# Kernel tuning notes

Hardware: AMD Instinct MI355X
Metric: run time of the kernel (lower is better)

The kernel has to match this reference:

```python
import jax, jax.numpy as jnp
import numpy as np

B = 500000
DT = 1.0

def _first_principles_A(dt):
    A = np.eye(8, dtype=np.float32)
    for i in range(4):
        A[i, i + 4] = dt
    return jnp.asarray(A)

def setup_inputs() -> dict:
    key = jax.random.key(0)
    k1, k2 = jax.random.split(key)
    # bbox-like state: keep positions/sizes positive so Q heuristic is sensible
    x = jax.random.uniform(k1, (B, 8, 1), dtype=jnp.float32, minval=0.1, maxval=1.0)
    P = jax.random.normal(k2, (B, 8, 8), dtype=jnp.float32) * 0.1
    A = _first_principles_A(DT)  # relu/triu leave it unchanged but we apply them anyway
    sigma_p = jnp.float32(0.05)
    sigma_v = jnp.float32(0.00625)
    return {"x": x, "P": P, "A": A, "sigma_p": sigma_p, "sigma_v": sigma_v}

def reference(x, P, A, sigma_p, sigma_v):
    # get_motion_matrix: relu then triu
    Ap = jnp.triu(jax.nn.relu(A))  # (8, 8)
    # x_hat = A @ x
    x_hat = jnp.einsum('ij,bjk->bik', Ap, x)  # (B, 8, 1)
    # process-noise heuristic: diag proportional to bbox h, w (x[:,2,0], x[:,3,0])
    h = x[:, 2, 0]
    w = x[:, 3, 0]
    xp, yp = h * sigma_p, w * sigma_p
    xv, yv = h * sigma_v, w * sigma_v
    diag = jnp.stack([xp, yp, xp, yp, xv, yv, xv, yv], axis=-1)  # (B, 8)
    Q = jnp.square(diag)[:, :, None] * jnp.eye(8, dtype=x.dtype)  # (B, 8, 8) diagonal
    # P_hat = A P A^T + Q
    P_hat = jnp.einsum('ij,bjk,lk->bil', Ap, P, Ap) + Q
    return (x_hat, P_hat)
```

## Files before the change

kernel.cpp:

```cpp
#include <hip/hip_runtime.h>


#define ROW_STRIDE 12
#define ELEM_STRIDE 100
#define ELEMS_PER_BLOCK 32

__device__ __align__(16) float g_cst[72];

__global__ void kalman_setup_kernel(const float* __restrict__ A,
                                    const float* __restrict__ sigp_ptr,
                                    const float* __restrict__ sigv_ptr)
{
    int t = threadIdx.x;
    if (t < 64) {
        float a = fmaxf(A[t], 0.0f);
        if ((t & 7) < (t >> 3)) a = 0.0f;
        g_cst[t] = a;
    }
    if (t < 8) g_cst[64 + t] = (t < 4) ? sigp_ptr[0] : sigv_ptr[0];
}

__global__ __launch_bounds__(256) void kalman_predict_kernel(
    const float* __restrict__ x,
    const float* __restrict__ P,
    float* __restrict__ x_hat,
    float* __restrict__ P_hat,
    int B)
{
    __shared__ float lds_m[ELEMS_PER_BLOCK * ELEM_STRIDE];

    int tid = blockIdx.x * blockDim.x + threadIdx.x;
    int e = tid >> 3;
    int r = tid & 7;
    int e_l = threadIdx.x >> 3;

    bool valid = (e < B);
    int e_c = valid ? e : (B - 1);

    unsigned poff = (unsigned)e_c * 64u + (unsigned)r * 8u;
    const float4* prow = (const float4*)(P + poff);
    float4 pa = prow[0], pb = prow[1];
    float p[8] = {pa.x, pa.y, pa.z, pa.w, pb.x, pb.y, pb.z, pb.w};

    const float4* xrow = (const float4*)(x + (unsigned)e_c * 8u);
    float4 x0 = xrow[0], x1 = xrow[1];
    float xv[8] = {x0.x, x0.y, x0.z, x0.w, x1.x, x1.y, x1.z, x1.w};

    float ap[64];
#pragma unroll
    for (int t = 0; t < 64; ++t) ap[t] = g_cst[t];

    const float4* arow = (const float4*)(g_cst + r * 8);
    float4 a0 = arow[0], a1 = arow[1];
    float apr[8] = {a0.x, a0.y, a0.z, a0.w, a1.x, a1.y, a1.z, a1.w};

    float sig = g_cst[64 + r];

    float m[8];
#pragma unroll
    for (int l = 0; l < 8; ++l) {
        float s = 0.0f;
#pragma unroll
        for (int k = l; k < 8; ++k) s = fmaf(ap[l * 8 + k], p[k], s);
        m[l] = s;
    }

    float* slot = lds_m + e_l * ELEM_STRIDE + r * ROW_STRIDE;
    ((float4*)slot)[0] = make_float4(m[0], m[1], m[2], m[3]);
    ((float4*)(slot + 4))[0] = make_float4(m[4], m[5], m[6], m[7]);

    asm volatile("s_waitcnt lgkmcnt(0)" ::: "memory");

    float hv = (r & 1) ? xv[3] : xv[2];
    float q = hv * sig;
    q = q * q;

    float xh = 0.0f;
#pragma unroll
    for (int j = 0; j < 8; ++j) xh = fmaf(apr[j], xv[j], xh);

    float out[8];
#pragma unroll
    for (int l = 0; l < 8; ++l) out[l] = (l == r) ? q : 0.0f;

    const float* ebase = lds_m + e_l * ELEM_STRIDE;
#pragma unroll
    for (int j = 0; j < 8; ++j) {
        const float4* mr = (const float4*)(ebase + j * ROW_STRIDE);
        float4 ma = mr[0], mb = mr[1];
        float mj[8] = {ma.x, ma.y, ma.z, ma.w, mb.x, mb.y, mb.z, mb.w};
#pragma unroll
        for (int l = 0; l < 8; ++l) out[l] = fmaf(apr[j], mj[l], out[l]);
    }

    if (valid) {
        x_hat[(unsigned)e * 8u + r] = xh;
        float4* po = (float4*)(P_hat + poff);
        po[0] = make_float4(out[0], out[1], out[2], out[3]);
        po[1] = make_float4(out[4], out[5], out[6], out[7]);
    }
}

extern "C" void kernel_launch(void* const* d_in, const int* in_sizes, int n_in,
                              void* d_out, int out_size, void* d_ws, size_t ws_size,
                              hipStream_t stream) {
    const float* x  = (const float*)d_in[0];
    const float* P  = (const float*)d_in[1];
    const float* A  = (const float*)d_in[2];
    const float* sp = (const float*)d_in[3];
    const float* sv = (const float*)d_in[4];

    int B = in_sizes[0] / 8;
    float* x_hat = (float*)d_out;
    float* P_hat = (float*)d_out + (size_t)B * 8;

    kalman_setup_kernel<<<1, 64, 0, stream>>>(A, sp, sv);

    int threads = B * 8;
    int block = 256;
    int grid = (threads + block - 1) / block;
    kalman_predict_kernel<<<grid, block, 0, stream>>>(x, P, x_hat, P_hat, B);
}
```

Measured before the change: 251.7 us.

## Process four elements per thread with hoisted loads and packed triangular constants

Each thread now handles four batch elements instead of one. All P and x loads for those elements are issued up front, before any compute, to raise memory-level parallelism. The grid shrinks by four, and the LDS slot is reused across the iterations. The upper-triangular motion matrix is also stored packed (36 values) alongside the full matrix, cutting per-thread constant loads and register use. The cost is more registers held for the outstanding loads and fewer waves in flight.

```diff
diff --git a/kernel.cpp b/kernel.cpp
--- a/kernel.cpp
+++ b/kernel.cpp
@@ -3,9 +3,10 @@
 
 #define ROW_STRIDE 12
 #define ELEM_STRIDE 100
-#define ELEMS_PER_BLOCK 32
+#define SLOTS 32
+#define EPT 4
 
-__device__ __align__(16) float g_cst[72];
+__device__ __align__(16) float g_cst[112];
 
 __global__ void kalman_setup_kernel(const float* __restrict__ A,
                                     const float* __restrict__ sigp_ptr,
@@ -13,11 +14,16 @@
 {
     int t = threadIdx.x;
     if (t < 64) {
+        int l = t >> 3, k = t & 7;
         float a = fmaxf(A[t], 0.0f);
-        if ((t & 7) < (t >> 3)) a = 0.0f;
-        g_cst[t] = a;
+        if (k < l) a = 0.0f;
+        g_cst[48 + t] = a;
+        if (k >= l) {
+            int off = l * 8 - (l * (l - 1)) / 2;
+            g_cst[off + (k - l)] = a;
+        }
     }
-    if (t < 8) g_cst[64 + t] = (t < 4) ? sigp_ptr[0] : sigv_ptr[0];
+    if (t < 8) g_cst[36 + t] = (t < 4) ? sigp_ptr[0] : sigv_ptr[0];
 }
 
 __global__ __launch_bounds__(256) void kalman_predict_kernel(
@@ -27,77 +33,90 @@
     float* __restrict__ P_hat,
     int B)
 {
-    __shared__ float lds_m[ELEMS_PER_BLOCK * ELEM_STRIDE];
+    __shared__ float lds_m[SLOTS * ELEM_STRIDE];
 
-    int tid = blockIdx.x * blockDim.x + threadIdx.x;
-    int e = tid >> 3;
-    int r = tid & 7;
+    int r   = threadIdx.x & 7;
     int e_l = threadIdx.x >> 3;
+    int eb  = blockIdx.x * (SLOTS * EPT);
 
-    bool valid = (e < B);
-    int e_c = valid ? e : (B - 1);
+    float4 pA[EPT], pB[EPT], xA[EPT], xB[EPT];
+    int ev[EPT];
+#pragma unroll
+    for (int i = 0; i < EPT; ++i) {
+        int e = eb + i * SLOTS + e_l;
+        ev[i] = e;
+        unsigned ec = (unsigned)((e < B) ? e : (B - 1));
+        const float4* prow = (const float4*)(P + (size_t)ec * 64u + (unsigned)r * 8u);
+        pA[i] = prow[0];
+        pB[i] = prow[1];
+        const float4* xrow = (const float4*)(x + (size_t)ec * 8u);
+        xA[i] = xrow[0];
+        xB[i] = xrow[1];
+    }
 
-    unsigned poff = (unsigned)e_c * 64u + (unsigned)r * 8u;
-    const float4* prow = (const float4*)(P + poff);
-    float4 pa = prow[0], pb = prow[1];
-    float p[8] = {pa.x, pa.y, pa.z, pa.w, pb.x, pb.y, pb.z, pb.w};
+    float apk[36];
+#pragma unroll
+    for (int t = 0; t < 36; ++t) apk[t] = g_cst[t];
 
-    const float4* xrow = (const float4*)(x + (unsigned)e_c * 8u);
-    float4 x0 = xrow[0], x1 = xrow[1];
-    float xv[8] = {x0.x, x0.y, x0.z, x0.w, x1.x, x1.y, x1.z, x1.w};
-
-    float ap[64];
-#pragma unroll
-    for (int t = 0; t < 64; ++t) ap[t] = g_cst[t];
-
-    const float4* arow = (const float4*)(g_cst + r * 8);
+    const float4* arow = (const float4*)(g_cst + 48 + r * 8);
     float4 a0 = arow[0], a1 = arow[1];
     float apr[8] = {a0.x, a0.y, a0.z, a0.w, a1.x, a1.y, a1.z, a1.w};
-
-    float sig = g_cst[64 + r];
-
-    float m[8];
-#pragma unroll
-    for (int l = 0; l < 8; ++l) {
-        float s = 0.0f;
-#pragma unroll
-        for (int k = l; k < 8; ++k) s = fmaf(ap[l * 8 + k], p[k], s);
-        m[l] = s;
-    }
+    float sig = g_cst[36 + r];
 
     float* slot = lds_m + e_l * ELEM_STRIDE + r * ROW_STRIDE;
-    ((float4*)slot)[0] = make_float4(m[0], m[1], m[2], m[3]);
-    ((float4*)(slot + 4))[0] = make_float4(m[4], m[5], m[6], m[7]);
+    const float* ebase = lds_m + e_l * ELEM_STRIDE;
 
-    asm volatile("s_waitcnt lgkmcnt(0)" ::: "memory");
+#pragma unroll
+    for (int i = 0; i < EPT; ++i) {
+        float p[8] = {pA[i].x, pA[i].y, pA[i].z, pA[i].w,
+                      pB[i].x, pB[i].y, pB[i].z, pB[i].w};
+        float xv[8] = {xA[i].x, xA[i].y, xA[i].z, xA[i].w,
+                       xB[i].x, xB[i].y, xB[i].z, xB[i].w};
 
-    float hv = (r & 1) ? xv[3] : xv[2];
-    float q = hv * sig;
-    q = q * q;
+        float m[8];
+        {
+            int idx = 0;
+#pragma unroll
+            for (int l = 0; l < 8; ++l) {
+                float s = 0.0f;
+#pragma unroll
+                for (int k = l; k < 8; ++k) s = fmaf(apk[idx + (k - l)], p[k], s);
+                m[l] = s;
+                idx += 8 - l;
+            }
+        }
 
-    float xh = 0.0f;
+        ((float4*)slot)[0] = make_float4(m[0], m[1], m[2], m[3]);
+        ((float4*)(slot + 4))[0] = make_float4(m[4], m[5], m[6], m[7]);
+        asm volatile("s_waitcnt lgkmcnt(0)" ::: "memory");
+
+        float hv = (r & 1) ? xv[3] : xv[2];
+        float q = hv * sig;
+        q = q * q;
+
+        float xh = 0.0f;
 #pragma unroll
-    for (int j = 0; j < 8; ++j) xh = fmaf(apr[j], xv[j], xh);
+        for (int j = 0; j < 8; ++j) xh = fmaf(apr[j], xv[j], xh);
 
-    float out[8];
+        float out[8];
 #pragma unroll
-    for (int l = 0; l < 8; ++l) out[l] = (l == r) ? q : 0.0f;
+        for (int l = 0; l < 8; ++l) out[l] = (l == r) ? q : 0.0f;
+#pragma unroll
+        for (int j = 0; j < 8; ++j) {
+            const float4* mr = (const float4*)(ebase + j * ROW_STRIDE);
+            float4 ma = mr[0], mb = mr[1];
+            float mj[8] = {ma.x, ma.y, ma.z, ma.w, mb.x, mb.y, mb.z, mb.w};
+#pragma unroll
+            for (int l = 0; l < 8; ++l) out[l] = fmaf(apr[j], mj[l], out[l]);
+        }
 
-    const float* ebase = lds_m + e_l * ELEM_STRIDE;
-#pragma unroll
-    for (int j = 0; j < 8; ++j) {
-        const float4* mr = (const float4*)(ebase + j * ROW_STRIDE);
-        float4 ma = mr[0], mb = mr[1];
-        float mj[8] = {ma.x, ma.y, ma.z, ma.w, mb.x, mb.y, mb.z, mb.w};
-#pragma unroll
-        for (int l = 0; l < 8; ++l) out[l] = fmaf(apr[j], mj[l], out[l]);
-    }
-
-    if (valid) {
-        x_hat[(unsigned)e * 8u + r] = xh;
-        float4* po = (float4*)(P_hat + poff);
-        po[0] = make_float4(out[0], out[1], out[2], out[3]);
-        po[1] = make_float4(out[4], out[5], out[6], out[7]);
+        if (ev[i] < B) {
+            unsigned e = (unsigned)ev[i];
+            x_hat[(size_t)e * 8u + r] = xh;
+            float4* po = (float4*)(P_hat + (size_t)e * 64u + (unsigned)r * 8u);
+            po[0] = make_float4(out[0], out[1], out[2], out[3]);
+            po[1] = make_float4(out[4], out[5], out[6], out[7]);
+        }
     }
 }
 
@@ -116,8 +135,7 @@
 
     kalman_setup_kernel<<<1, 64, 0, stream>>>(A, sp, sv);
 
-    int threads = B * 8;
-    int block = 256;
-    int grid = (threads + block - 1) / block;
-    kalman_predict_kernel<<<grid, block, 0, stream>>>(x, P, x_hat, P_hat, B);
+    int elems_per_block = SLOTS * EPT;
+    int grid = (B + elems_per_block - 1) / elems_per_block;
+    kalman_predict_kernel<<<grid, 256, 0, stream>>>(x, P, x_hat, P_hat, B);
 }
```

Measured after the change: 256.8 us. 2.0% more time.
